# Kernel optimization log

Hardware: AMD Instinct MI355X
Metric: run time of the kernel (lower is better)

The kernel has to match this reference:

```python
import jax, jax.numpy as jnp
import numpy as np

HEADS = 8
DIM_HEAD = 64
EPS = 1e-4
SCALE = DIM_HEAD ** -0.5


def setup_inputs() -> dict:
    key = jax.random.key(0)
    k1, k2, k3, k4 = jax.random.split(key, 4)
    dim = HEADS * DIM_HEAD  # 512
    x = jax.random.normal(k1, (2, 2048, dim), dtype=jnp.float32)
    # torch Linear weights are [out, in]; scale like default init
    Wq = jax.random.normal(k2, (dim, dim), dtype=jnp.float32) / np.sqrt(dim)
    Wkv = jax.random.normal(k3, (2 * dim, dim), dtype=jnp.float32) / np.sqrt(dim)
    Wout = jax.random.normal(k4, (dim, dim), dtype=jnp.float32) / np.sqrt(dim)
    return {"x": x, "Wq": Wq, "Wkv": Wkv, "Wout": Wout}


def _normalize_magnitude(t, eps=EPS):
    # divide by (sqrt(mean(t^2, -1)) + eps)
    mag = jnp.sqrt(jnp.mean(t * t, axis=-1, keepdims=True)) + eps
    return t / mag


def reference(x, Wq, Wkv, Wout):
    b, n, dim = x.shape
    h, d = HEADS, DIM_HEAD
    # norm=False -> Identity; context = x (self-attention)
    q = x @ Wq.T                      # [b, n, h*d]
    kv = x @ Wkv.T                    # [b, n, 2*h*d]
    k, v = jnp.split(kv, 2, axis=-1)
    def to_heads(t):
        return t.reshape(b, n, h, d).transpose(0, 2, 1, 3)  # [b, h, n, d]
    q, k, v = map(to_heads, (q, k, v))
    q = _normalize_magnitude(q)
    k = _normalize_magnitude(k)
    sim = jnp.einsum('bhid,bhjd->bhij', q, k) * SCALE
    attn = jax.nn.softmax(sim, axis=-1)
    out = jnp.einsum('bhij,bhjd->bhid', attn, v)
    out = out.transpose(0, 2, 1, 3).reshape(b, n, h * d)
    return out @ Wout.T
```

## Files before the change

### kernel.cpp

```cpp
#include <hip/hip_runtime.h>

typedef __bf16 bf16x8 __attribute__((ext_vector_type(8)));
typedef __bf16 bf16x4 __attribute__((ext_vector_type(4)));
typedef float  f32x4  __attribute__((ext_vector_type(4)));

#define LOG2E_F 1.44269504088896340736f

static constexpr int kB = 2, kN = 2048, kH = 8, kD = 64, kDim = 512;
static constexpr int kTok = kB * kN;
static constexpr int kNQKV = 1536;
static constexpr int kKH = 4;

__device__ __forceinline__ void gld16(const void* g, void* l) {
  __builtin_amdgcn_global_load_lds(
      (const __attribute__((address_space(1))) void*)g,
      (__attribute__((address_space(3))) void*)l, 16, 0, 0);
}

__global__ __launch_bounds__(256) void cvt_all(const float* __restrict__ x,
                                               const float* __restrict__ wq,
                                               const float* __restrict__ wkv,
                                               const float* __restrict__ wo,
                                               __bf16* __restrict__ xb,
                                               __bf16* __restrict__ wqkvb,
                                               __bf16* __restrict__ wob) {
  size_t i = ((size_t)blockIdx.x * 256 + threadIdx.x) * 8;
  const float* s; __bf16* d; size_t off;
  if (i < 2097152)      { s = x;   d = xb;              off = i; }
  else if (i < 2359296) { s = wq;  d = wqkvb;           off = i - 2097152; }
  else if (i < 2883584) { s = wkv; d = wqkvb + 262144;  off = i - 2359296; }
  else                  { s = wo;  d = wob;             off = i - 2883584; }
  float4 u = *(const float4*)(s + off);
  float4 v = *(const float4*)(s + off + 4);
  bf16x8 t;
  t[0] = (__bf16)u.x; t[1] = (__bf16)u.y; t[2] = (__bf16)u.z; t[3] = (__bf16)u.w;
  t[4] = (__bf16)v.x; t[5] = (__bf16)v.y; t[6] = (__bf16)v.z; t[7] = (__bf16)v.w;
  *(bf16x8*)(d + off) = t;
}

__global__ __launch_bounds__(256, 3) void gemm_qkv(const __bf16* __restrict__ A,
                                                   const __bf16* __restrict__ B,
                                                   __bf16* __restrict__ qn,
                                                   __bf16* __restrict__ kn,
                                                   __bf16* __restrict__ vt2) {
  const int K = kDim;
  const int tid = threadIdx.x;
  const int w = tid >> 6, lane = tid & 63, quad = lane >> 4, lq = lane & 15;
  const int m0 = blockIdx.y * 128;
  const int n0 = blockIdx.x * 64;
  const int wm = w * 32;
  __shared__ __bf16 As[2][128 * 64];
  __shared__ __bf16 Bs[2][64 * 64];

  const f32x4 zero = {0.f, 0.f, 0.f, 0.f};
  f32x4 acc[2][4];
#pragma unroll
  for (int fm = 0; fm < 2; ++fm)
#pragma unroll
    for (int fn = 0; fn < 4; ++fn) acc[fm][fn] = zero;

  const int sr = tid >> 3, sc = (tid & 7) << 3;
  auto stage = [&](int k0, int buf) {
#pragma unroll
    for (int j = 0; j < 4; ++j)
      gld16(A + (size_t)(m0 + j * 32 + sr) * K + k0 + sc,
            &As[buf][(size_t)(j * 32 + sr) * 64 + sc]);
#pragma unroll
    for (int j = 0; j < 2; ++j)
      gld16(B + (size_t)(n0 + j * 32 + sr) * K + k0 + sc,
            &Bs[buf][(size_t)(j * 32 + sr) * 64 + sc]);
  };

  stage(0, 0);
  for (int i = 0; i < 8; ++i) {
    __syncthreads();
    if (i + 1 < 8) stage((i + 1) << 6, (i + 1) & 1);
    const __bf16* as = As[i & 1];
    const __bf16* bs = Bs[i & 1];
#pragma unroll
    for (int ks = 0; ks < 2; ++ks) {
      bf16x8 a[2], b[4];
#pragma unroll
      for (int fm = 0; fm < 2; ++fm)
        a[fm] = *(const bf16x8*)&as[(wm + fm * 16 + lq) * 64 + ks * 32 + quad * 8];
#pragma unroll
      for (int fn = 0; fn < 4; ++fn)
        b[fn] = *(const bf16x8*)&bs[(fn * 16 + lq) * 64 + ks * 32 + quad * 8];
#pragma unroll
      for (int fm = 0; fm < 2; ++fm)
#pragma unroll
        for (int fn = 0; fn < 4; ++fn)
          acc[fm][fn] =
              __builtin_amdgcn_mfma_f32_16x16x32_bf16(a[fm], b[fn], acc[fm][fn], 0, 0, 0);
    }
  }

  const int h = (n0 >> 6) & 7;
  if (n0 >= 1024) {
    __syncthreads();
    __bf16* Ts = &As[0][0];
#pragma unroll
    for (int fm = 0; fm < 2; ++fm)
#pragma unroll
      for (int r = 0; r < 4; ++r) {
        const int mo = wm + fm * 16 + quad * 4 + r;
        const int tau = mo >> 6, tt = mo & 63;
        const int p = (tt & 15) * 4 + (tt >> 4);
#pragma unroll
        for (int fn = 0; fn < 4; ++fn)
          Ts[tau * 4608 + (fn * 16 + lq) * 72 + p] = (__bf16)acc[fm][fn][r];
      }
    __syncthreads();
    const int b = m0 >> 11, kt0 = (m0 & (kN - 1)) >> 6;
    const int dd = tid >> 2, p0 = (tid & 3) << 4;
#pragma unroll
    for (int tau = 0; tau < 2; ++tau) {
      const __bf16* src = Ts + tau * 4608 + dd * 72 + p0;
      __bf16* dst = vt2 + ((size_t)((b * kH + h) * 32 + kt0 + tau)) * 4096 + tid * 16;
      *(bf16x8*)dst = *(const bf16x8*)src;
      *(bf16x8*)(dst + 8) = *(const bf16x8*)(src + 8);
    }
  } else {
    const float qs = (n0 < 512) ? (0.125f * LOG2E_F) : 1.0f;
    __bf16* dst0 = (n0 < 512) ? qn : kn;
#pragma unroll
    for (int fm = 0; fm < 2; ++fm)
#pragma unroll
      for (int r = 0; r < 4; ++r) {
        float ss = 0.f;
#pragma unroll
        for (int fn = 0; fn < 4; ++fn) ss += acc[fm][fn][r] * acc[fm][fn][r];
#pragma unroll
        for (int off = 1; off < 16; off <<= 1) ss += __shfl_xor(ss, off, 64);
        const float inv = qs / (sqrtf(ss * (1.f / 64)) + 1e-4f);
        const int m = m0 + wm + fm * 16 + quad * 4 + r;
        const int b = m >> 11, n = m & (kN - 1);
        __bf16* dst = dst0 + ((size_t)(b * kH + h) * kN + n) * kD;
#pragma unroll
        for (int fn = 0; fn < 4; ++fn)
          dst[fn * 16 + lq] = (__bf16)(acc[fm][fn][r] * inv);
      }
  }
}

__global__ __launch_bounds__(256, 2) void attn(const __bf16* __restrict__ qn,
                                               const __bf16* __restrict__ kn,
                                               const __bf16* __restrict__ vt2,
                                               __bf16* __restrict__ po,
                                               float* __restrict__ pl) {
  const int qt = blockIdx.x, bh = blockIdx.y, kh = blockIdx.z;
  const int tid = threadIdx.x;
  const int w = tid >> 6, lane = tid & 63, quad = lane >> 4, lq = lane & 15;
  __shared__ __bf16 Ks[2][4096];
  __shared__ __bf16 Vs[2][4096];
  __shared__ __bf16 Ps[4][32 * 72];
  __bf16* myP = Ps[w];

  bf16x8 aq[2][2];
#pragma unroll
  for (int fm = 0; fm < 2; ++fm) {
    const __bf16* Qb = qn + ((size_t)bh * kN + qt * 128 + w * 32 + fm * 16 + lq) * kD;
    aq[fm][0] = *(const bf16x8*)(Qb + quad * 8);
    aq[fm][1] = *(const bf16x8*)(Qb + 32 + quad * 8);
  }

  const f32x4 zero  = {0.f, 0.f, 0.f, 0.f};
  const f32x4 minit = {-12.f, -12.f, -12.f, -12.f};
  f32x4 o[2][4];
  float lr[2][4];
#pragma unroll
  for (int fm = 0; fm < 2; ++fm)
#pragma unroll
    for (int i = 0; i < 4; ++i) { o[fm][i] = zero; lr[fm][i] = 0.f; }

  const __bf16* Kb = kn + ((size_t)bh * kN + kh * 512) * kD;
  const __bf16* Vb = vt2 + (size_t)(bh * 32 + kh * 8) * 4096;

  auto stage = [&](int kt, int buf) {
#pragma unroll
    for (int j = 0; j < 2; ++j) {
      gld16(Kb + (size_t)kt * 4096 + (j * 256 + tid) * 8, &Ks[buf][(j * 256 + tid) * 8]);
      gld16(Vb + (size_t)kt * 4096 + (j * 256 + tid) * 8, &Vs[buf][(j * 256 + tid) * 8]);
    }
  };

  stage(0, 0);
#pragma unroll 2
  for (int kt = 0; kt < 8; ++kt) {
    __syncthreads();
    if (kt < 7) stage(kt + 1, (kt + 1) & 1);
    const __bf16* ks_ = Ks[kt & 1];
    const __bf16* vs_ = Vs[kt & 1];

    bf16x8 kb0[4], kb1[4], vb0[4], vb1[4];
#pragma unroll
    for (int fn = 0; fn < 4; ++fn) {
      const int row = fn * 16 + lq;
      kb0[fn] = *(const bf16x8*)&ks_[row * 64 + quad * 8];
      kb1[fn] = *(const bf16x8*)&ks_[row * 64 + 32 + quad * 8];
      vb0[fn] = *(const bf16x8*)&vs_[row * 64 + quad * 8];
      vb1[fn] = *(const bf16x8*)&vs_[row * 64 + 32 + quad * 8];
    }
    f32x4 s[2][4];
#pragma unroll
    for (int fm = 0; fm < 2; ++fm)
#pragma unroll
      for (int fn = 0; fn < 4; ++fn) {
        f32x4 a = __builtin_amdgcn_mfma_f32_16x16x32_bf16(aq[fm][0], kb0[fn], minit, 0, 0, 0);
        s[fm][fn] = __builtin_amdgcn_mfma_f32_16x16x32_bf16(aq[fm][1], kb1[fn], a, 0, 0, 0);
      }

#pragma unroll
    for (int fm = 0; fm < 2; ++fm)
#pragma unroll
      for (int r = 0; r < 4; ++r) {
        const float p0 = __builtin_amdgcn_exp2f(s[fm][0][r]);
        const float p1 = __builtin_amdgcn_exp2f(s[fm][1][r]);
        const float p2 = __builtin_amdgcn_exp2f(s[fm][2][r]);
        const float p3 = __builtin_amdgcn_exp2f(s[fm][3][r]);
        lr[fm][r] += (p0 + p1) + (p2 + p3);
        bf16x4 pk = {(__bf16)p0, (__bf16)p1, (__bf16)p2, (__bf16)p3};
        *(bf16x4*)&myP[(fm * 16 + quad * 4 + r) * 72 + lq * 4] = pk;
      }

#pragma unroll
    for (int fm = 0; fm < 2; ++fm) {
      bf16x8 ap0 = *(const bf16x8*)&myP[(fm * 16 + lq) * 72 + quad * 8];
      bf16x8 ap1 = *(const bf16x8*)&myP[(fm * 16 + lq) * 72 + 32 + quad * 8];
#pragma unroll
      for (int fn = 0; fn < 4; ++fn) {
        o[fm][fn] = __builtin_amdgcn_mfma_f32_16x16x32_bf16(ap0, vb0[fn], o[fm][fn], 0, 0, 0);
        o[fm][fn] = __builtin_amdgcn_mfma_f32_16x16x32_bf16(ap1, vb1[fn], o[fm][fn], 0, 0, 0);
      }
    }
  }

  const int b = bh >> 3, h = bh & 7;
#pragma unroll
  for (int fm = 0; fm < 2; ++fm) {
    const int qrow0 = qt * 128 + w * 32 + fm * 16 + quad * 4;
#pragma unroll
    for (int r = 0; r < 4; ++r) {
      float sum = lr[fm][r];
#pragma unroll
      for (int off = 1; off < 16; off <<= 1) sum += __shfl_xor(sum, off, 64);
      if (lq == 0) pl[(size_t)kh * 32768 + bh * kN + qrow0 + r] = sum;
      const size_t ob = ((size_t)kh * kTok + b * kN + qrow0 + r) * kDim + h * 64;
#pragma unroll
      for (int fn = 0; fn < 4; ++fn) po[ob + fn * 16 + lq] = (__bf16)o[fm][fn][r];
    }
  }
}

__global__ __launch_bounds__(256) void combine(const __bf16* __restrict__ po,
                                               const float* __restrict__ pl,
                                               __bf16* __restrict__ ao) {
  const size_t i = ((size_t)blockIdx.x * 256 + threadIdx.x) * 4;
  const int tok = (int)(i >> 9), dk = (int)(i & 511);
  const int h = dk >> 6, b = tok >> 11, qrow = tok & (kN - 1);
  const int idx = (b * kH + h) * kN + qrow;
  float l = 0.f;
#pragma unroll
  for (int kh = 0; kh < kKH; ++kh) l += pl[kh * 32768 + idx];
  const float inv = 1.f / l;
  float s0 = 0.f, s1 = 0.f, s2 = 0.f, s3 = 0.f;
#pragma unroll
  for (int kh = 0; kh < kKH; ++kh) {
    bf16x4 a = *(const bf16x4*)(po + (size_t)kh * kTok * kDim + i);
    s0 += (float)a[0]; s1 += (float)a[1]; s2 += (float)a[2]; s3 += (float)a[3];
  }
  bf16x4 t = {(__bf16)(s0 * inv), (__bf16)(s1 * inv),
              (__bf16)(s2 * inv), (__bf16)(s3 * inv)};
  *(bf16x4*)(ao + i) = t;
}

__global__ __launch_bounds__(256, 2) void gemm64(const __bf16* __restrict__ A,
                                                 const __bf16* __restrict__ B,
                                                 float* __restrict__ C,
                                                 int N, int K) {
  const int tid = threadIdx.x;
  const int w = tid >> 6, lane = tid & 63, quad = lane >> 4, lq = lane & 15;
  const int m0 = blockIdx.y * 64;
  const int n0 = blockIdx.x * 64;
  const int wm = (w >> 1) * 32, wn = (w & 1) * 32;
  __shared__ __bf16 As[2][4096];
  __shared__ __bf16 Bs[2][4096];

  const f32x4 zero = {0.f, 0.f, 0.f, 0.f};
  f32x4 acc00 = zero, acc01 = zero, acc10 = zero, acc11 = zero;

  const int sr = tid >> 3, sc = (tid & 7) << 3;
  auto stage = [&](int k0, int buf) {
#pragma unroll
    for (int j = 0; j < 2; ++j) {
      gld16(A + (size_t)(m0 + j * 32 + sr) * K + k0 + sc,
            &As[buf][(j * 32 + sr) * 64 + sc]);
      gld16(B + (size_t)(n0 + j * 32 + sr) * K + k0 + sc,
            &Bs[buf][(j * 32 + sr) * 64 + sc]);
    }
  };

  stage(0, 0);
  const int iters = K >> 6;
  for (int i = 0; i < iters; ++i) {
    __syncthreads();
    if (i + 1 < iters) stage((i + 1) << 6, (i + 1) & 1);
    const __bf16* as = As[i & 1];
    const __bf16* bs = Bs[i & 1];
#pragma unroll
    for (int ks = 0; ks < 2; ++ks) {
      bf16x8 a0 = *(const bf16x8*)&as[(wm +      lq) * 64 + ks * 32 + quad * 8];
      bf16x8 a1 = *(const bf16x8*)&as[(wm + 16 + lq) * 64 + ks * 32 + quad * 8];
      bf16x8 b0 = *(const bf16x8*)&bs[(wn +      lq) * 64 + ks * 32 + quad * 8];
      bf16x8 b1 = *(const bf16x8*)&bs[(wn + 16 + lq) * 64 + ks * 32 + quad * 8];
      acc00 = __builtin_amdgcn_mfma_f32_16x16x32_bf16(a0, b0, acc00, 0, 0, 0);
      acc01 = __builtin_amdgcn_mfma_f32_16x16x32_bf16(a0, b1, acc01, 0, 0, 0);
      acc10 = __builtin_amdgcn_mfma_f32_16x16x32_bf16(a1, b0, acc10, 0, 0, 0);
      acc11 = __builtin_amdgcn_mfma_f32_16x16x32_bf16(a1, b1, acc11, 0, 0, 0);
    }
  }
  const f32x4 av[2][2] = {{acc00, acc01}, {acc10, acc11}};
#pragma unroll
  for (int fm = 0; fm < 2; ++fm)
#pragma unroll
    for (int fn = 0; fn < 2; ++fn)
#pragma unroll
      for (int r = 0; r < 4; ++r)
        C[(size_t)(m0 + wm + fm * 16 + quad * 4 + r) * N + (n0 + wn + fn * 16 + lq)] =
            av[fm][fn][r];
}

extern "C" void kernel_launch(void* const* d_in, const int* in_sizes, int n_in,
                              void* d_out, int out_size, void* d_ws, size_t ws_size,
                              hipStream_t stream) {
  const float* x    = (const float*)d_in[0];
  const float* Wq   = (const float*)d_in[1];
  const float* Wkv  = (const float*)d_in[2];
  const float* Wout = (const float*)d_in[3];
  float* out = (float*)d_out;
  char* ws = (char*)d_ws;

  __bf16* xb    = (__bf16*)(ws);
  __bf16* wqkvb = (__bf16*)(ws + (size_t)(4 << 20));
  __bf16* wob   = (__bf16*)(ws + (size_t)(6 << 20));
  __bf16* qn    = (__bf16*)(ws + (size_t)(7 << 20));
  __bf16* kn    = (__bf16*)(ws + (size_t)(11 << 20));
  __bf16* vt2   = (__bf16*)(ws + (size_t)(15 << 20));
  __bf16* po    = (__bf16*)(ws + (size_t)(19 << 20));
  float*  pl    = (float*)(ws + (size_t)(35 << 20));
  __bf16* ao    = (__bf16*)(ws + (size_t)(36 << 20));

  cvt_all<<<1536, 256, 0, stream>>>(x, Wq, Wkv, Wout, xb, wqkvb, wob);
  gemm_qkv<<<dim3(kNQKV / 64, kTok / 128), 256, 0, stream>>>(xb, wqkvb, qn, kn, vt2);
  attn<<<dim3(kN / 128, kB * kH, kKH), 256, 0, stream>>>(qn, kn, vt2, po, pl);
  combine<<<kTok * kDim / 1024, 256, 0, stream>>>(po, pl, ao);
  gemm64<<<dim3(kDim / 64, kTok / 64), 256, 0, stream>>>(ao, wob, out, kDim, kDim);
}
```

Baseline: 129.7 us.

## Swizzle LDS tiles to avoid bank conflicts and split attention keys three ways

Applies an XOR swizzle to the shared-memory layout of the A/B tiles in both GEMMs and the K/V tiles in attention, to remove LDS bank conflicts on the 16-byte fragment reads. Attention now splits the key range into 3 chunks of 11/11/10 tiles instead of 4 equal chunks and raises the occupancy hint to 3 blocks per CU. This reduces partial outputs and combine work but gives uneven chunk lengths and more register pressure. Workspace offsets are compacted to match the smaller partial buffer.

```diff
diff --git a/kernel.cpp b/kernel.cpp
--- a/kernel.cpp
+++ b/kernel.cpp
@@ -9,13 +9,14 @@
 static constexpr int kB = 2, kN = 2048, kH = 8, kD = 64, kDim = 512;
 static constexpr int kTok = kB * kN;
 static constexpr int kNQKV = 1536;
-static constexpr int kKH = 4;
+static constexpr int kKH = 3;
 
 __device__ __forceinline__ void gld16(const void* g, void* l) {
   __builtin_amdgcn_global_load_lds(
       (const __attribute__((address_space(1))) void*)g,
       (__attribute__((address_space(3))) void*)l, 16, 0, 0);
 }
+
 
 __global__ __launch_bounds__(256) void cvt_all(const float* __restrict__ x,
                                                const float* __restrict__ wq,
@@ -59,17 +60,23 @@
 #pragma unroll
     for (int fn = 0; fn < 4; ++fn) acc[fm][fn] = zero;
 
-  const int sr = tid >> 3, sc = (tid & 7) << 3;
+  const int sr = tid >> 3, ch = tid & 7;
   auto stage = [&](int k0, int buf) {
 #pragma unroll
-    for (int j = 0; j < 4; ++j)
-      gld16(A + (size_t)(m0 + j * 32 + sr) * K + k0 + sc,
-            &As[buf][(size_t)(j * 32 + sr) * 64 + sc]);
-#pragma unroll
-    for (int j = 0; j < 2; ++j)
-      gld16(B + (size_t)(n0 + j * 32 + sr) * K + k0 + sc,
-            &Bs[buf][(size_t)(j * 32 + sr) * 64 + sc]);
+    for (int j = 0; j < 4; ++j) {
+      const int row = j * 32 + sr;
+      gld16(A + (size_t)(m0 + row) * K + k0 + ((ch ^ (row & 7)) << 3),
+            &As[buf][row * 64 + ch * 8]);
+    }
+#pragma unroll
+    for (int j = 0; j < 2; ++j) {
+      const int row = j * 32 + sr;
+      gld16(B + (size_t)(n0 + row) * K + k0 + ((ch ^ (row & 7)) << 3),
+            &Bs[buf][row * 64 + ch * 8]);
+    }
   };
+  const int sw0 = ((quad ^ (lq & 7)) << 3);
+  const int sw1 = (((4 | quad) ^ (lq & 7)) << 3);
 
   stage(0, 0);
   for (int i = 0; i < 8; ++i) {
@@ -79,13 +86,14 @@
     const __bf16* bs = Bs[i & 1];
 #pragma unroll
     for (int ks = 0; ks < 2; ++ks) {
+      const int sw = ks ? sw1 : sw0;
       bf16x8 a[2], b[4];
 #pragma unroll
       for (int fm = 0; fm < 2; ++fm)
-        a[fm] = *(const bf16x8*)&as[(wm + fm * 16 + lq) * 64 + ks * 32 + quad * 8];
+        a[fm] = *(const bf16x8*)&as[(wm + fm * 16 + lq) * 64 + sw];
 #pragma unroll
       for (int fn = 0; fn < 4; ++fn)
-        b[fn] = *(const bf16x8*)&bs[(fn * 16 + lq) * 64 + ks * 32 + quad * 8];
+        b[fn] = *(const bf16x8*)&bs[(fn * 16 + lq) * 64 + sw];
 #pragma unroll
       for (int fm = 0; fm < 2; ++fm)
 #pragma unroll
@@ -143,12 +151,14 @@
   }
 }
 
-__global__ __launch_bounds__(256, 2) void attn(const __bf16* __restrict__ qn,
+__global__ __launch_bounds__(256, 3) void attn(const __bf16* __restrict__ qn,
                                                const __bf16* __restrict__ kn,
                                                const __bf16* __restrict__ vt2,
                                                __bf16* __restrict__ po,
                                                float* __restrict__ pl) {
   const int qt = blockIdx.x, bh = blockIdx.y, kh = blockIdx.z;
+  const int kt0 = kh * 11;
+  const int cnt = (kh == 2) ? 10 : 11;
   const int tid = threadIdx.x;
   const int w = tid >> 6, lane = tid & 63, quad = lane >> 4, lq = lane & 15;
   __shared__ __bf16 Ks[2][4096];
@@ -173,33 +183,37 @@
 #pragma unroll
     for (int i = 0; i < 4; ++i) { o[fm][i] = zero; lr[fm][i] = 0.f; }
 
-  const __bf16* Kb = kn + ((size_t)bh * kN + kh * 512) * kD;
-  const __bf16* Vb = vt2 + (size_t)(bh * 32 + kh * 8) * 4096;
-
-  auto stage = [&](int kt, int buf) {
+  const __bf16* Kb = kn + (size_t)bh * kN * kD;
+  const __bf16* Vb = vt2 + (size_t)bh * 32 * 4096;
+
+  auto stage = [&](int ktg, int buf) {
 #pragma unroll
     for (int j = 0; j < 2; ++j) {
-      gld16(Kb + (size_t)kt * 4096 + (j * 256 + tid) * 8, &Ks[buf][(j * 256 + tid) * 8]);
-      gld16(Vb + (size_t)kt * 4096 + (j * 256 + tid) * 8, &Vs[buf][(j * 256 + tid) * 8]);
+      const int s = j * 256 + tid;
+      const int row = s >> 3, ch = s & 7;
+      const int src = row * 64 + ((ch ^ (row & 7)) << 3);
+      gld16(Kb + (size_t)ktg * 4096 + src, &Ks[buf][s * 8]);
+      gld16(Vb + (size_t)ktg * 4096 + src, &Vs[buf][s * 8]);
     }
   };
-
-  stage(0, 0);
-#pragma unroll 2
-  for (int kt = 0; kt < 8; ++kt) {
-    __syncthreads();
-    if (kt < 7) stage(kt + 1, (kt + 1) & 1);
+  const int sw0 = ((quad ^ (lq & 7)) << 3);
+  const int sw1 = (((4 | quad) ^ (lq & 7)) << 3);
+
+  stage(kt0, 0);
+  for (int kt = 0; kt < cnt; ++kt) {
+    __syncthreads();
+    if (kt + 1 < cnt) stage(kt0 + kt + 1, (kt + 1) & 1);
     const __bf16* ks_ = Ks[kt & 1];
     const __bf16* vs_ = Vs[kt & 1];
 
     bf16x8 kb0[4], kb1[4], vb0[4], vb1[4];
 #pragma unroll
     for (int fn = 0; fn < 4; ++fn) {
-      const int row = fn * 16 + lq;
-      kb0[fn] = *(const bf16x8*)&ks_[row * 64 + quad * 8];
-      kb1[fn] = *(const bf16x8*)&ks_[row * 64 + 32 + quad * 8];
-      vb0[fn] = *(const bf16x8*)&vs_[row * 64 + quad * 8];
-      vb1[fn] = *(const bf16x8*)&vs_[row * 64 + 32 + quad * 8];
+      const int rb = (fn * 16 + lq) * 64;
+      kb0[fn] = *(const bf16x8*)&ks_[rb + sw0];
+      kb1[fn] = *(const bf16x8*)&ks_[rb + sw1];
+      vb0[fn] = *(const bf16x8*)&vs_[rb + sw0];
+      vb1[fn] = *(const bf16x8*)&vs_[rb + sw1];
     }
     f32x4 s[2][4];
 #pragma unroll
@@ -289,16 +303,18 @@
   const f32x4 zero = {0.f, 0.f, 0.f, 0.f};
   f32x4 acc00 = zero, acc01 = zero, acc10 = zero, acc11 = zero;
 
-  const int sr = tid >> 3, sc = (tid & 7) << 3;
+  const int sr = tid >> 3, ch = tid & 7;
   auto stage = [&](int k0, int buf) {
 #pragma unroll
     for (int j = 0; j < 2; ++j) {
-      gld16(A + (size_t)(m0 + j * 32 + sr) * K + k0 + sc,
-            &As[buf][(j * 32 + sr) * 64 + sc]);
-      gld16(B + (size_t)(n0 + j * 32 + sr) * K + k0 + sc,
-            &Bs[buf][(j * 32 + sr) * 64 + sc]);
+      const int row = j * 32 + sr;
+      const int src = k0 + ((ch ^ (row & 7)) << 3);
+      gld16(A + (size_t)(m0 + row) * K + src, &As[buf][row * 64 + ch * 8]);
+      gld16(B + (size_t)(n0 + row) * K + src, &Bs[buf][row * 64 + ch * 8]);
     }
   };
+  const int sw0 = ((quad ^ (lq & 7)) << 3);
+  const int sw1 = (((4 | quad) ^ (lq & 7)) << 3);
 
   stage(0, 0);
   const int iters = K >> 6;
@@ -309,10 +325,11 @@
     const __bf16* bs = Bs[i & 1];
 #pragma unroll
     for (int ks = 0; ks < 2; ++ks) {
-      bf16x8 a0 = *(const bf16x8*)&as[(wm +      lq) * 64 + ks * 32 + quad * 8];
-      bf16x8 a1 = *(const bf16x8*)&as[(wm + 16 + lq) * 64 + ks * 32 + quad * 8];
-      bf16x8 b0 = *(const bf16x8*)&bs[(wn +      lq) * 64 + ks * 32 + quad * 8];
-      bf16x8 b1 = *(const bf16x8*)&bs[(wn + 16 + lq) * 64 + ks * 32 + quad * 8];
+      const int sw = ks ? sw1 : sw0;
+      bf16x8 a0 = *(const bf16x8*)&as[(wm +      lq) * 64 + sw];
+      bf16x8 a1 = *(const bf16x8*)&as[(wm + 16 + lq) * 64 + sw];
+      bf16x8 b0 = *(const bf16x8*)&bs[(wn +      lq) * 64 + sw];
+      bf16x8 b1 = *(const bf16x8*)&bs[(wn + 16 + lq) * 64 + sw];
       acc00 = __builtin_amdgcn_mfma_f32_16x16x32_bf16(a0, b0, acc00, 0, 0, 0);
       acc01 = __builtin_amdgcn_mfma_f32_16x16x32_bf16(a0, b1, acc01, 0, 0, 0);
       acc10 = __builtin_amdgcn_mfma_f32_16x16x32_bf16(a1, b0, acc10, 0, 0, 0);
@@ -347,8 +364,8 @@
   __bf16* kn    = (__bf16*)(ws + (size_t)(11 << 20));
   __bf16* vt2   = (__bf16*)(ws + (size_t)(15 << 20));
   __bf16* po    = (__bf16*)(ws + (size_t)(19 << 20));
-  float*  pl    = (float*)(ws + (size_t)(35 << 20));
-  __bf16* ao    = (__bf16*)(ws + (size_t)(36 << 20));
+  float*  pl    = (float*)(ws + (size_t)(32 << 20));
+  __bf16* ao    = (__bf16*)(ws + (size_t)(33 << 20));
 
   cvt_all<<<1536, 256, 0, stream>>>(x, Wq, Wkv, Wout, xb, wqkvb, wob);
   gemm_qkv<<<dim3(kNQKV / 64, kTok / 128), 256, 0, stream>>>(xb, wqkvb, qn, kn, vt2);
```

After: 118.3 us. 8.8% less time.
